# Optimization experiments

Measured on AMD Instinct MI355X. Metric: run time of the kernel, lower is better.

Reference implementation:

```python
import jax, jax.numpy as jnp
import numpy as np

N = 20000   # nodes per type per hop
E = 200000  # edges per relation per hop
H = 512     # node_feature_hid_len
FU = 512    # raw user feature len
FI = 256    # raw item feature len
NUM_RES = 2
NUM_DNN = 2


def setup_inputs() -> dict:
    key = jax.random.key(0)
    ks = iter(jax.random.split(key, 64))
    p = lambda shape: jax.random.normal(next(ks), shape, dtype=jnp.float32) * 0.05
    inp = {}
    # features per hop per type
    for h in range(3):
        inp[f'feat_user_h{h}'] = jax.random.normal(next(ks), (N, FU), dtype=jnp.float32)
        inp[f'feat_item_h{h}'] = jax.random.normal(next(ks), (N, FI), dtype=jnp.float32)
    del inp['feat_user_h2_']; 


def _unused():
    pass

# rebuild setup_inputs cleanly (above stub replaced)

def setup_inputs() -> dict:
    key = jax.random.key(0)
    ks = iter(jax.random.split(key, 64))
    p = lambda shape: jax.random.normal(next(ks), shape, dtype=jnp.float32) * 0.05
    inp = {}
    for h in range(3):
        inp[f'feat_user_h{h}'] = jax.random.normal(next(ks), (N, FU), dtype=jnp.float32)
        inp[f'feat_item_h{h}'] = jax.random.normal(next(ks), (N, FI), dtype=jnp.float32)
    for name in ('edges_UI_h0', 'edges_IU_h0', 'edges_UI_h1', 'edges_IU_h1'):
        inp[name] = jax.random.randint(next(ks), (2, E), 0, N, dtype=jnp.int32)
    # per-node-type input transforms
    inp['W_user'] = p((FU, H)); inp['b_user'] = jnp.zeros((H,), jnp.float32)
    inp['W_item'] = p((FI, H)); inp['b_item'] = jnp.zeros((H,), jnp.float32)
    # per-relation GATConv params, stacked over 2 relations [UI, IU]
    inp['gat_feat_W'] = p((2, H, H)); inp['gat_feat_b'] = jnp.zeros((2, H), jnp.float32)
    inp['gat_att_w'] = p((2, 2 * H)); inp['gat_att_b'] = jnp.zeros((2,), jnp.float32)
    inp['gat_bias'] = jnp.zeros((2, H), jnp.float32)
    # Res_DNN params
    inp['prep_W'] = p((H, H)); inp['prep_b'] = jnp.zeros((H,), jnp.float32)
    inp['dnn_W'] = p((NUM_RES, NUM_DNN, H, H)); inp['dnn_b'] = jnp.zeros((NUM_RES, NUM_DNN, H), jnp.float32)
    inp['dnn_ln_g'] = jnp.ones((NUM_RES, NUM_DNN, H), jnp.float32); inp['dnn_ln_b'] = jnp.zeros((NUM_RES, NUM_DNN, H), jnp.float32)
    inp['res_ln_g'] = jnp.ones((NUM_RES, H), jnp.float32); inp['res_ln_b'] = jnp.zeros((NUM_RES, H), jnp.float32)
    inp['cls_W'] = p((H, 1)); inp['cls_b'] = jnp.zeros((1,), jnp.float32)
    return inp


def _ln(x, g, b, eps=1e-5):
    mu = jnp.mean(x, axis=-1, keepdims=True)
    var = jnp.mean((x - mu) ** 2, axis=-1, keepdims=True)
    return (x - mu) * jax.lax.rsqrt(var + eps) * g + b


def _gat(head_h, tail_h, edges, fW, fb, aw, ab, bias):
    # GATConv: feat_linear on both sides, tanh edge attention, per-source-row
    # sparse softmax, scatter-weighted sum of transformed tail features.
    s = head_h @ fW + fb            # [Nh, H]
    t = tail_h @ fW + fb            # [Nt, H]
    src, tgt = edges[0], edges[1]
    # att(cat([s_e, t_e])) split into per-node scores (same math as concat @ aw)
    e = jnp.tanh((s @ aw[:H])[src] + (t @ aw[H:])[tgt] + ab)  # [E]
    nh = head_h.shape[0]
    m = jax.ops.segment_max(e, src, num_segments=nh)
    ex = jnp.exp(e - m[src])
    den = jax.ops.segment_sum(ex, src, num_segments=nh)
    alpha = ex / den[src]
    hp = jax.ops.segment_sum(alpha[:, None] * t[tgt], src, num_segments=nh)
    return hp + bias


def _forward(feat_user_h0, feat_item_h0, feat_user_h1, feat_item_h1,
             feat_user_h2, feat_item_h2,
             W_user, b_user, W_item, b_item,
             gat_feat_W, gat_feat_b, gat_att_w, gat_att_b, gat_bias,
             prep_W, prep_b, dnn_W, dnn_b, dnn_ln_g, dnn_ln_b,
             res_ln_g, res_ln_b, cls_W, cls_b,
             edges_UI_h0, edges_IU_h0, edges_UI_h1, edges_IU_h1):
    def gat(r, head, tail, edges):
        return _gat(head, tail, edges, gat_feat_W[r], gat_feat_b[r],
                    gat_att_w[r], gat_att_b[r], gat_bias[r])
    # hop 2 (deepest): transformed source features
    su = feat_user_h2 @ W_user + b_user
    si = feat_item_h2 @ W_item + b_item
    # hop 1
    hu = feat_user_h1 @ W_user + b_user
    hi = feat_item_h1 @ W_item + b_item
    su_new = (hu + gat(0, hu, si, edges_UI_h1)) * 0.5  # mean of [self, UI agg]
    si_new = (hi + gat(1, hi, su, edges_IU_h1)) * 0.5
    su, si = su_new, si_new
    # hop 0
    hu = feat_user_h0 @ W_user + b_user
    hi = feat_item_h0 @ W_item + b_item
    su_new = (hu + gat(0, hu, si, edges_UI_h0)) * 0.5
    su = su_new  # target node type = 'user' (first key)
    # Res_DNN head
    x = su @ prep_W + prep_b
    for r in range(NUM_RES):
        sc = x
        for d in range(NUM_DNN):
            x = _ln(jnp.tanh(x @ dnn_W[r, d] + dnn_b[r, d]), dnn_ln_g[r, d], dnn_ln_b[r, d])
        x = _ln(jnp.tanh(sc + x), res_ln_g[r], res_ln_b[r])
    return jax.nn.sigmoid(x @ cls_W + cls_b)  # [N, 1]


def reference(feat_user_h0, feat_item_h0, feat_user_h1, feat_item_h1,
              feat_user_h2, feat_item_h2,
              edges_UI_h0, edges_IU_h0, edges_UI_h1, edges_IU_h1,
              W_user, b_user, W_item, b_item,
              gat_feat_W, gat_feat_b, gat_att_w, gat_att_b, gat_bias,
              prep_W, prep_b, dnn_W, dnn_b, dnn_ln_g, dnn_ln_b,
              res_ln_g, res_ln_b, cls_W, cls_b):
    return _forward(feat_user_h0, feat_item_h0, feat_user_h1, feat_item_h1,
                    feat_user_h2, feat_item_h2,
                    W_user, b_user, W_item, b_item,
                    gat_feat_W, gat_feat_b, gat_att_w, gat_att_b, gat_bias,
                    prep_W, prep_b, dnn_W, dnn_b, dnn_ln_g, dnn_ln_b,
                    res_ln_g, res_ln_b, cls_W, cls_b,
                    edges_UI_h0, edges_IU_h0, edges_UI_h1, edges_IU_h1)
```

## Files before the change

kernel.cpp:

```cpp
#include <hip/hip_runtime.h>
#include <math.h>

#define NN 20000
#define NE 200000
#define HH 512

typedef __attribute__((ext_vector_type(8))) short short8v;
typedef __attribute__((ext_vector_type(4))) float f32x4;

__device__ inline short f2bf(float f) {
    union { float f; unsigned u; } v; v.f = f;
    unsigned r = (v.u + 0x7fffu + ((v.u >> 16) & 1u)) >> 16;
    return (short)r;
}
__device__ inline float bf2f(short s) {
    union { unsigned u; float f; } v;
    v.u = ((unsigned)(unsigned short)s) << 16;
    return v.f;
}

__device__ inline void gload_lds16(const void* g, void* l) {
    __builtin_amdgcn_global_load_lds(
        (const __attribute__((address_space(1))) void*)g,
        (__attribute__((address_space(3))) void*)l, 16, 0, 0);
}

__global__ __launch_bounds__(256)
void f2b_kernel(const float* __restrict__ src, short* __restrict__ dst, int n8)
{
    int i = blockIdx.x * 256 + threadIdx.x;
    if (i >= n8) return;
    const float4* p = (const float4*)src + (size_t)i * 2;
    float4 a = p[0], b = p[1];
    short8v s;
    s[0] = f2bf(a.x); s[1] = f2bf(a.y); s[2] = f2bf(a.z); s[3] = f2bf(a.w);
    s[4] = f2bf(b.x); s[5] = f2bf(b.y); s[6] = f2bf(b.z); s[7] = f2bf(b.w);
    ((short8v*)dst)[i] = s;
}

__global__ __launch_bounds__(256)
void wtr_kernel(const float* __restrict__ src, short* __restrict__ dst,
                int K, int Ncols)
{
    __shared__ float t[32][33];
    int bx = blockIdx.x * 32;
    int by = blockIdx.y * 32;
    int tx = threadIdx.x, ty = threadIdx.y;
    for (int i = ty; i < 32; i += 8)
        t[i][tx] = src[(size_t)(by + i) * Ncols + bx + tx];
    __syncthreads();
    for (int i = ty; i < 32; i += 8)
        dst[(size_t)(bx + i) * K + by + tx] = f2bf(t[tx][i]);
}

__global__ __launch_bounds__(256)
void mfma_lin(const short* __restrict__ X, const short* __restrict__ WT,
              const float* __restrict__ bias, float* __restrict__ outF,
              short* __restrict__ outB, int M, int K)
{
    __shared__ short8v pool[3072];

    const int tid = threadIdx.x;
    const int lane = tid & 63;
    const int w = tid >> 6;

    const int nby = (M + 127) >> 7;
    const int nwg = nby << 2;
    const int q = nwg >> 3, r = nwg & 7;
    int id = blockIdx.x;
    int xcd = id & 7, wi = id >> 3;
    int wgid = (xcd < r ? xcd * (q + 1) : r * (q + 1) + (xcd - r) * q) + wi;
    const int col0 = (wgid & 3) * 128;
    const int row0 = (wgid >> 2) * 128;

    const int wr = (w >> 1) * 64;
    const int wc = (w & 1) * 64;

    int sp0 = w * 128 + lane;
    int sp1 = sp0 + 64;
    int r0_ = sp0 >> 2, r1_ = sp1 >> 2;
    int c0_ = (sp0 & 3) ^ ((r0_ >> 1) & 3);
    int c1_ = (sp1 & 3) ^ ((r1_ >> 1) & 3);
    int ga0 = row0 + r0_; if (ga0 >= M) ga0 = M - 1;
    int ga1 = row0 + r1_; if (ga1 >= M) ga1 = M - 1;
    const short* ag0 = X + (size_t)ga0 * K + c0_ * 8;
    const short* ag1 = X + (size_t)ga1 * K + c1_ * 8;
    const short* bg0 = WT + (size_t)(col0 + r0_) * K + c0_ * 8;
    const short* bg1 = WT + (size_t)(col0 + r1_) * K + c1_ * 8;

    int ar[4], br[4];
#pragma unroll
    for (int i = 0; i < 4; ++i) {
        int rr = wr + i * 16 + (lane & 15);
        ar[i] = rr * 4 + ((lane >> 4) ^ ((rr >> 1) & 3));
        int nn = wc + i * 16 + (lane & 15);
        br[i] = nn * 4 + ((lane >> 4) ^ ((nn >> 1) & 3));
    }

    f32x4 acc[4][4];
#pragma unroll
    for (int i = 0; i < 4; ++i)
#pragma unroll
        for (int j = 0; j < 4; ++j)
            acc[i][j] = (f32x4){0.f, 0.f, 0.f, 0.f};

    auto stage = [&](int buf, int kk) {
        short8v* A = pool + buf * 512;
        short8v* B = pool + 1536 + buf * 512;
        gload_lds16(ag0 + kk, A + w * 128);
        gload_lds16(ag1 + kk, A + w * 128 + 64);
        gload_lds16(bg0 + kk, B + w * 128);
        gload_lds16(bg1 + kk, B + w * 128 + 64);
    };

    const int nt = K >> 5;
    stage(0, 0);
    if (nt > 1) stage(1, 32);
    if (nt > 2) stage(2, 64);
    int cur = 0;
    for (int t = 0; t < nt; ++t) {
        if (t + 2 < nt)      asm volatile("s_waitcnt vmcnt(8)" ::: "memory");
        else if (t + 1 < nt) asm volatile("s_waitcnt vmcnt(4)" ::: "memory");
        else                 asm volatile("s_waitcnt vmcnt(0)" ::: "memory");
        __builtin_amdgcn_s_barrier();
        const short8v* A = pool + cur * 512;
        const short8v* B = pool + 1536 + cur * 512;
        short8v af[4], bf[4];
#pragma unroll
        for (int i = 0; i < 4; ++i) af[i] = A[ar[i]];
#pragma unroll
        for (int j = 0; j < 4; ++j) bf[j] = B[br[j]];
#pragma unroll
        for (int i = 0; i < 4; ++i)
#pragma unroll
            for (int j = 0; j < 4; ++j)
                acc[i][j] = __builtin_amdgcn_mfma_f32_16x16x32_bf16(af[i], bf[j], acc[i][j], 0, 0, 0);
        __builtin_amdgcn_s_barrier();
        if (t + 3 < nt) stage(cur, (t + 3) * 32);
        cur = (cur == 2) ? 0 : cur + 1;
    }

    float bj[4];
#pragma unroll
    for (int j = 0; j < 4; ++j)
        bj[j] = bias[col0 + wc + j * 16 + (lane & 15)];

    if (outF) {
#pragma unroll
        for (int i = 0; i < 4; ++i) {
#pragma unroll
            for (int rr = 0; rr < 4; ++rr) {
                int row = row0 + wr + i * 16 + (lane >> 4) * 4 + rr;
                if (row < M) {
                    float* op = outF + (size_t)row * HH + col0 + wc + (lane & 15);
#pragma unroll
                    for (int j = 0; j < 4; ++j) op[j * 16] = acc[i][j][rr] + bj[j];
                }
            }
        }
    }
    if (outB) {
        short* lds = (short*)pool + w * 4608;
#pragma unroll
        for (int i = 0; i < 4; ++i)
#pragma unroll
            for (int rr = 0; rr < 4; ++rr) {
                int lrow = i * 16 + (lane >> 4) * 4 + rr;
#pragma unroll
                for (int j = 0; j < 4; ++j)
                    lds[lrow * 72 + j * 16 + (lane & 15)] = f2bf(acc[i][j][rr] + bj[j]);
            }
#pragma unroll
        for (int k = 0; k < 8; ++k) {
            int lr = (lane >> 3) + 8 * k;
            int lc = (lane & 7) * 8;
            int grow = row0 + wr + lr;
            if (grow < M) {
                short8v vv = *(short8v*)(lds + lr * 72 + lc);
                *(short8v*)(outB + (size_t)grow * HH + col0 + wc + lc) = vv;
            }
        }
    }
}

__global__ __launch_bounds__(256)
void gat_pre_kernel(const float* __restrict__ fW, const float* __restrict__ fb,
                    const float* __restrict__ aw, float* __restrict__ uv,
                    float* __restrict__ s0t0)
{
    int row = blockIdx.x * 4 + (threadIdx.x >> 6);
    int lane = threadIdx.x & 63;
    const float4* ah = (const float4*)aw;
    const float4* at = (const float4*)(aw + HH);
    const float4* fp;
    if (row < 512)      fp = (const float4*)(fW + (size_t)row * HH);
    else if (row == 512) fp = (const float4*)fb;
    else return;
    float du = 0.f, dv = 0.f;
#pragma unroll
    for (int l = 0; l < 2; ++l) {
        int idx = lane * 2 + l;
        float4 f = fp[idx], a = ah[idx], b = at[idx];
        du += f.x*a.x + f.y*a.y + f.z*a.z + f.w*a.w;
        dv += f.x*b.x + f.y*b.y + f.z*b.z + f.w*b.w;
    }
#pragma unroll
    for (int m = 32; m >= 1; m >>= 1) {
        du += __shfl_xor(du, m);
        dv += __shfl_xor(dv, m);
    }
    if (lane == 0) {
        if (row < 512) { uv[row] = du; uv[512 + row] = dv; }
        else           { s0t0[0] = du; s0t0[1] = dv; }
    }
}

__global__ __launch_bounds__(256)
void rowdot2_kernel(const short* __restrict__ Hd, const short* __restrict__ Tl,
                    const float* __restrict__ uv, const float* __restrict__ s0t0,
                    float* __restrict__ ss, float* __restrict__ ts, int N)
{
    int row = blockIdx.x * 4 + (threadIdx.x >> 6);
    int lane = threadIdx.x & 63;
    if (row >= N) return;
    short8v h = ((const short8v*)(Hd + (size_t)row * HH))[lane];
    short8v t = ((const short8v*)(Tl + (size_t)row * HH))[lane];
    const float4* up = (const float4*)uv + lane * 2;
    const float4* vp = (const float4*)(uv + HH) + lane * 2;
    float4 u0 = up[0], u1 = up[1], v0 = vp[0], v1 = vp[1];
    float a = bf2f(h[0])*u0.x + bf2f(h[1])*u0.y + bf2f(h[2])*u0.z + bf2f(h[3])*u0.w
            + bf2f(h[4])*u1.x + bf2f(h[5])*u1.y + bf2f(h[6])*u1.z + bf2f(h[7])*u1.w;
    float b = bf2f(t[0])*v0.x + bf2f(t[1])*v0.y + bf2f(t[2])*v0.z + bf2f(t[3])*v0.w
            + bf2f(t[4])*v1.x + bf2f(t[5])*v1.y + bf2f(t[6])*v1.z + bf2f(t[7])*v1.w;
#pragma unroll
    for (int m = 32; m >= 1; m >>= 1) {
        a += __shfl_xor(a, m);
        b += __shfl_xor(b, m);
    }
    if (lane == 0) { ss[row] = a + s0t0[0]; ts[row] = b + s0t0[1]; }
}

__global__ __launch_bounds__(256)
void count2_kernel(const int* __restrict__ s0, const int* __restrict__ s1,
                   int* __restrict__ c0, int* __restrict__ c1, int E)
{
    int i = blockIdx.x * blockDim.x + threadIdx.x;
    if (i < E) atomicAdd(&c0[s0[i]], 1);
    else if (i < 2 * E) atomicAdd(&c1[s1[i - E]], 1);
}

__global__ __launch_bounds__(1024)
void scan2_kernel(const int* __restrict__ c0, const int* __restrict__ c1,
                  int* __restrict__ o0, int* __restrict__ o1,
                  int* __restrict__ u0, int* __restrict__ u1, int n)
{
    const int* counts = blockIdx.x ? c1 : c0;
    int* offs = blockIdx.x ? o1 : o0;
    int* curs = blockIdx.x ? u1 : u0;
    __shared__ int part[1024];
    const int tid = threadIdx.x;
    const int CH = (n + 1023) / 1024;
    const int base = tid * CH;
    int s = 0;
    for (int i = 0; i < CH; ++i) {
        int idx = base + i;
        if (idx < n) s += counts[idx];
    }
    part[tid] = s;
    __syncthreads();
    for (int d = 1; d < 1024; d <<= 1) {
        int v = 0;
        if (tid >= d) v = part[tid - d];
        __syncthreads();
        if (tid >= d) part[tid] += v;
        __syncthreads();
    }
    int run = (tid == 0) ? 0 : part[tid - 1];
    for (int i = 0; i < CH; ++i) {
        int idx = base + i;
        if (idx < n) { offs[idx] = run; curs[idx] = run; run += counts[idx]; }
    }
    if (tid == 1023) offs[n] = run;
}

__global__ __launch_bounds__(256)
void fill_kernel(const int* __restrict__ src, const int* __restrict__ tgt,
                 const float* __restrict__ ss, const float* __restrict__ ts,
                 const float* __restrict__ ab_ptr, int* __restrict__ cursor,
                 int* __restrict__ tvals, float* __restrict__ wv, int E)
{
    int i = blockIdx.x * blockDim.x + threadIdx.x;
    if (i >= E) return;
    int s = src[i], t = tgt[i];
    int pos = atomicAdd(&cursor[s], 1);
    tvals[pos] = t;
    wv[pos] = expf(tanhf(ss[s] + ts[t] + ab_ptr[0]));
}

__global__ __launch_bounds__(256)
void gat_agg_kernel(const int* __restrict__ offs, const int* __restrict__ tvals,
                    const float* __restrict__ wv, const short* __restrict__ T,
                    const short* __restrict__ head, const float* __restrict__ gbias,
                    short* __restrict__ out, int N)
{
    int s = blockIdx.x * 4 + (threadIdx.x >> 6);
    int lane = threadIdx.x & 63;
    if (s >= N) return;
    const int beg = offs[s], end = offs[s + 1];
    float a[8];
#pragma unroll
    for (int q = 0; q < 8; ++q) a[q] = 0.f;
    float den = 0.f;

    int j = beg;
    for (; j + 4 <= end; j += 4) {
        int t0 = tvals[j], t1 = tvals[j + 1], t2 = tvals[j + 2], t3 = tvals[j + 3];
        float w0 = wv[j], w1 = wv[j + 1], w2 = wv[j + 2], w3 = wv[j + 3];
        short8v v0 = ((const short8v*)(T + (size_t)t0 * HH))[lane];
        short8v v1 = ((const short8v*)(T + (size_t)t1 * HH))[lane];
        short8v v2 = ((const short8v*)(T + (size_t)t2 * HH))[lane];
        short8v v3 = ((const short8v*)(T + (size_t)t3 * HH))[lane];
        den += w0 + w1 + w2 + w3;
#pragma unroll
        for (int q = 0; q < 8; ++q) {
            float acc = a[q];
            acc = fmaf(w0, bf2f(v0[q]), acc);
            acc = fmaf(w1, bf2f(v1[q]), acc);
            acc = fmaf(w2, bf2f(v2[q]), acc);
            acc = fmaf(w3, bf2f(v3[q]), acc);
            a[q] = acc;
        }
    }
    for (; j < end; ++j) {
        int t = tvals[j];
        float w = wv[j];
        short8v tv = ((const short8v*)(T + (size_t)t * HH))[lane];
        den += w;
#pragma unroll
        for (int q = 0; q < 8; ++q) a[q] = fmaf(w, bf2f(tv[q]), a[q]);
    }
    float inv = (den > 0.f) ? 1.f / den : 0.f;

    short8v h = ((const short8v*)(head + (size_t)s * HH))[lane];
    const float4* bp = (const float4*)gbias + lane * 2;
    float4 b0 = bp[0], b1 = bp[1];
    float bb[8] = {b0.x, b0.y, b0.z, b0.w, b1.x, b1.y, b1.z, b1.w};
    short8v o;
#pragma unroll
    for (int q = 0; q < 8; ++q)
        o[q] = f2bf((bf2f(h[q]) + a[q] * inv + bb[q]) * 0.5f);
    ((short8v*)(out + (size_t)s * HH))[lane] = o;
}

__global__ __launch_bounds__(256)
void tanh_ln_kernel(const short* __restrict__ Z, const float* __restrict__ res,
                    const float* __restrict__ g, const float* __restrict__ bta,
                    short* __restrict__ outB, float* __restrict__ outF,
                    const float* __restrict__ cWp, const float* __restrict__ cbp,
                    float* __restrict__ outCls, int N)
{
    int row = blockIdx.x * 4 + (threadIdx.x >> 6);
    int lane = threadIdx.x & 63;
    if (row >= N) return;
    short8v zv = ((const short8v*)(Z + (size_t)row * HH))[lane];
    float v[8];
    float sum = 0.f, sum2 = 0.f;
    float rr[8];
    if (res) {
        const float4* rp = (const float4*)(res + (size_t)row * HH) + lane * 2;
        float4 r0 = rp[0], r1 = rp[1];
        rr[0]=r0.x; rr[1]=r0.y; rr[2]=r0.z; rr[3]=r0.w;
        rr[4]=r1.x; rr[5]=r1.y; rr[6]=r1.z; rr[7]=r1.w;
    } else {
#pragma unroll
        for (int q = 0; q < 8; ++q) rr[q] = 0.f;
    }
#pragma unroll
    for (int q = 0; q < 8; ++q) {
        float t = tanhf(bf2f(zv[q]) + rr[q]);
        v[q] = t;
        sum += t;
        sum2 = fmaf(t, t, sum2);
    }
#pragma unroll
    for (int m = 32; m >= 1; m >>= 1) {
        sum  += __shfl_xor(sum, m);
        sum2 += __shfl_xor(sum2, m);
    }
    float mu  = sum * (1.f/HH);
    float var = sum2 * (1.f/HH) - mu*mu;
    float rs  = rsqrtf(var + 1e-5f);
    const float4* gp = (const float4*)g + lane * 2;
    const float4* bp = (const float4*)bta + lane * 2;
    float4 g0 = gp[0], g1 = gp[1], c0 = bp[0], c1 = bp[1];
    float gg[8] = {g0.x, g0.y, g0.z, g0.w, g1.x, g1.y, g1.z, g1.w};
    float cc[8] = {c0.x, c0.y, c0.z, c0.w, c1.x, c1.y, c1.z, c1.w};
    float o[8];
#pragma unroll
    for (int q = 0; q < 8; ++q) o[q] = (v[q]-mu)*rs*gg[q] + cc[q];
    if (outB) {
        short8v ob;
#pragma unroll
        for (int q = 0; q < 8; ++q) ob[q] = f2bf(o[q]);
        ((short8v*)(outB + (size_t)row * HH))[lane] = ob;
    }
    if (outF) {
        float4* op = (float4*)(outF + (size_t)row * HH) + lane * 2;
        op[0] = make_float4(o[0], o[1], o[2], o[3]);
        op[1] = make_float4(o[4], o[5], o[6], o[7]);
    }
    if (cWp) {
        const float4* wp = (const float4*)cWp + lane * 2;
        float4 w0 = wp[0], w1 = wp[1];
        float acc = o[0]*w0.x + o[1]*w0.y + o[2]*w0.z + o[3]*w0.w
                  + o[4]*w1.x + o[5]*w1.y + o[6]*w1.z + o[7]*w1.w;
#pragma unroll
        for (int m = 32; m >= 1; m >>= 1) acc += __shfl_xor(acc, m);
        if (lane == 0) outCls[row] = 1.f / (1.f + expf(-(acc + cbp[0])));
    }
}

extern "C" void kernel_launch(void* const* d_in, const int* in_sizes, int n_in,
                              void* d_out, int out_size, void* d_ws, size_t ws_size,
                              hipStream_t stream)
{
    (void)in_sizes; (void)n_in; (void)out_size; (void)ws_size;
    const int N = NN, E = NE, H = HH;
    const size_t NHf = (size_t)N * H;

    const float* fu0 = (const float*)d_in[0];
    const float* fi1 = (const float*)d_in[3];
    const float* fu2 = (const float*)d_in[4];
    const int* eUI0 = (const int*)d_in[6];
    const int* eIU1 = (const int*)d_in[9];
    const float* Wu  = (const float*)d_in[10];
    const float* bu  = (const float*)d_in[11];
    const float* Wi  = (const float*)d_in[12];
    const float* bi  = (const float*)d_in[13];
    const float* gfW = (const float*)d_in[14];
    const float* gfb = (const float*)d_in[15];
    const float* gaw = (const float*)d_in[16];
    const float* gab = (const float*)d_in[17];
    const float* gbias = (const float*)d_in[18];
    const float* prW = (const float*)d_in[19];
    const float* prb = (const float*)d_in[20];
    const float* dW  = (const float*)d_in[21];
    const float* db  = (const float*)d_in[22];
    const float* dlg = (const float*)d_in[23];
    const float* dlb = (const float*)d_in[24];
    const float* rlg = (const float*)d_in[25];
    const float* rlb = (const float*)d_in[26];
    const float* cW  = (const float*)d_in[27];
    const float* cb  = (const float*)d_in[28];

    float* B5   = (float*)d_ws;
    float* ssb  = B5 + NHf;
    float* tsb  = ssb + N;
    float* uv   = tsb + N;
    float* s0t0 = uv + 1024;
    float* wvb  = s0t0 + 4;
    int* counts0 = (int*)(wvb + E);
    int* counts1 = counts0 + N;
    int* offs0   = counts1 + N;
    int* offs1   = offs0 + N + 1;
    int* cur0    = offs1 + N + 1;
    int* cur1    = cur0 + N;
    int* tvals   = cur1 + N;
    size_t boff = (size_t)((char*)(tvals + E) - (char*)d_ws);
    boff = (boff + 15) & ~(size_t)15;
    short* S0    = (short*)((char*)d_ws + boff);
    short* SUHU  = S0 + 2 * NHf;
    short* XI1   = SUHU + 2 * NHf;
    short* HI    = XI1 + NHf / 2;
    short* SINEW = HI + NHf;
    short* T4    = SINEW + NHf;
    short* SUF   = T4 + NHf;
    short* WTu   = SUF + NHf;
    short* WTi   = WTu + 512 * 512;
    short* WTg0  = WTi + 512 * 256;
    short* WTg1  = WTg0 + 512 * 512;
    short* WTpr  = WTg1 + 512 * 512;
    short* WTd   = WTpr + 512 * 512;
    short* SU  = SUHU;
    short* HU0 = SUHU + NHf;
    short* XB  = SINEW;
    short* ZB  = SU;

    auto WTR = [&](const float* src, short* dst, int K) {
        hipLaunchKernelGGL(wtr_kernel, dim3(16, K / 32), dim3(32, 8), 0, stream,
                           src, dst, K, 512);
    };
    WTR(Wu, WTu, 512);
    WTR(Wi, WTi, 256);
    WTR(gfW, WTg0, 512);
    WTR(gfW + (size_t)H * H, WTg1, 512);
    WTR(prW, WTpr, 512);
    for (int k = 0; k < 4; ++k)
        WTR(dW + (size_t)k * H * H, WTd + (size_t)k * 512 * 512, 512);

    auto F2B = [&](const float* src, short* dst, size_t n) {
        int n8 = (int)(n / 8);
        hipLaunchKernelGGL(f2b_kernel, dim3((n8 + 255) / 256), dim3(256), 0, stream,
                           src, dst, n8);
    };

    hipMemsetAsync(counts0, 0, 2 * N * sizeof(int), stream);
    hipLaunchKernelGGL(count2_kernel, dim3((2 * E + 255) / 256), dim3(256), 0, stream,
                       eUI0, eIU1, counts0, counts1, E);
    hipLaunchKernelGGL(scan2_kernel, dim3(2), dim3(1024), 0, stream,
                       counts0, counts1, offs0, offs1, cur0, cur1, N);

    auto MLIN = [&](const short* X, const short* WT, const float* b,
                    float* oF, short* oB, int M, int K) {
        int nwg = ((M + 127) / 128) * 4;
        hipLaunchKernelGGL(mfma_lin, dim3(nwg), dim3(256), 0, stream,
                           X, WT, b, oF, oB, M, K);
    };
    const int rgrid = (N + 3) / 4;
    const int egrid = (E + 255) / 256;

    auto GAT = [&](int r, const short* headB, const short* tailB, const short* WTg,
                   const int* edges, int* offs, int* curs, short* outB) {
        hipLaunchKernelGGL(gat_pre_kernel, dim3(130), dim3(256), 0, stream,
                           gfW + (size_t)r * H * H, gfb + r * H, gaw + (size_t)r * 2 * H,
                           uv, s0t0);
        MLIN(tailB, WTg, gfb + r * H, nullptr, T4, N, 512);
        hipLaunchKernelGGL(rowdot2_kernel, dim3(rgrid), dim3(256), 0, stream,
                           headB, tailB, uv, s0t0, ssb, tsb, N);
        hipLaunchKernelGGL(fill_kernel, dim3(egrid), dim3(256), 0, stream,
                           edges, edges + E, ssb, tsb, gab + r, curs, tvals, wvb, E);
        hipLaunchKernelGGL(gat_agg_kernel, dim3(rgrid), dim3(256), 0, stream,
                           offs, tvals, wvb, T4, headB, gbias + (size_t)r * H, outB, N);
    };

    F2B(fu2, S0, NHf);
    F2B(fu0, S0 + NHf, NHf);
    F2B(fi1, XI1, NHf / 2);
    MLIN(S0, WTu, bu, nullptr, SUHU, 2 * N, 512);
    MLIN(XI1, WTi, bi, nullptr, HI, N, 256);
    GAT(1, HI, SU, WTg1, eIU1, offs1, cur1, SINEW);
    GAT(0, HU0, SINEW, WTg0, eUI0, offs0, cur0, SUF);

    MLIN(SUF, WTpr, prb, B5, XB, N, 512);
    for (int r = 0; r < 2; ++r) {
        for (int d = 0; d < 2; ++d) {
            MLIN(XB, WTd + (size_t)(r * 2 + d) * 512 * 512, db + (r * 2 + d) * H,
                 nullptr, ZB, N, 512);
            hipLaunchKernelGGL(tanh_ln_kernel, dim3(rgrid), dim3(256), 0, stream,
                               ZB, (const float*)nullptr, dlg + (r * 2 + d) * H,
                               dlb + (r * 2 + d) * H, XB, (float*)nullptr,
                               (const float*)nullptr, (const float*)nullptr,
                               (float*)nullptr, N);
        }
        if (r == 0) {
            hipLaunchKernelGGL(tanh_ln_kernel, dim3(rgrid), dim3(256), 0, stream,
                               XB, B5, rlg, rlb, XB, B5,
                               (const float*)nullptr, (const float*)nullptr,
                               (float*)nullptr, N);
        } else {
            hipLaunchKernelGGL(tanh_ln_kernel, dim3(rgrid), dim3(256), 0, stream,
                               XB, B5, rlg + H, rlb + H, (short*)nullptr,
                               (float*)nullptr, cW, cb, (float*)d_out, N);
        }
    }
}
```

Baseline: 571.7 us.

## Shrink GEMM tile to 128x64 with four 32-row warps for more workgroups

```diff
diff --git a/kernel.cpp b/kernel.cpp
--- a/kernel.cpp
+++ b/kernel.cpp
@@ -58,59 +58,62 @@
               const float* __restrict__ bias, float* __restrict__ outF,
               short* __restrict__ outB, int M, int K)
 {
-    __shared__ short8v pool[3072];
+    __shared__ short8v pool[2304];
 
     const int tid = threadIdx.x;
     const int lane = tid & 63;
     const int w = tid >> 6;
 
     const int nby = (M + 127) >> 7;
-    const int nwg = nby << 2;
+    const int nwg = nby << 3;
     const int q = nwg >> 3, r = nwg & 7;
     int id = blockIdx.x;
     int xcd = id & 7, wi = id >> 3;
     int wgid = (xcd < r ? xcd * (q + 1) : r * (q + 1) + (xcd - r) * q) + wi;
-    const int col0 = (wgid & 3) * 128;
-    const int row0 = (wgid >> 2) * 128;
-
-    const int wr = (w >> 1) * 64;
-    const int wc = (w & 1) * 64;
-
-    int sp0 = w * 128 + lane;
-    int sp1 = sp0 + 64;
-    int r0_ = sp0 >> 2, r1_ = sp1 >> 2;
-    int c0_ = (sp0 & 3) ^ ((r0_ >> 1) & 3);
-    int c1_ = (sp1 & 3) ^ ((r1_ >> 1) & 3);
-    int ga0 = row0 + r0_; if (ga0 >= M) ga0 = M - 1;
-    int ga1 = row0 + r1_; if (ga1 >= M) ga1 = M - 1;
-    const short* ag0 = X + (size_t)ga0 * K + c0_ * 8;
-    const short* ag1 = X + (size_t)ga1 * K + c1_ * 8;
-    const short* bg0 = WT + (size_t)(col0 + r0_) * K + c0_ * 8;
-    const short* bg1 = WT + (size_t)(col0 + r1_) * K + c1_ * 8;
-
-    int ar[4], br[4];
-#pragma unroll
-    for (int i = 0; i < 4; ++i) {
-        int rr = wr + i * 16 + (lane & 15);
+    const int col0 = (wgid & 7) * 64;
+    const int row0 = (wgid >> 3) * 128;
+
+    const short* gsrc[3];
+#pragma unroll
+    for (int g = 0; g < 3; ++g) {
+        int p = w * 192 + g * 64 + lane;
+        if (p < 512) {
+            int row = p >> 2;
+            int c = (p & 3) ^ ((row >> 1) & 3);
+            int ga = row0 + row; if (ga >= M) ga = M - 1;
+            gsrc[g] = X + (size_t)ga * K + c * 8;
+        } else {
+            int qq = p - 512;
+            int col = qq >> 2;
+            int c = (qq & 3) ^ ((col >> 1) & 3);
+            gsrc[g] = WT + (size_t)(col0 + col) * K + c * 8;
+        }
+    }
+
+    int ar[2], br[4];
+#pragma unroll
+    for (int i = 0; i < 2; ++i) {
+        int rr = w * 32 + i * 16 + (lane & 15);
         ar[i] = rr * 4 + ((lane >> 4) ^ ((rr >> 1) & 3));
-        int nn = wc + i * 16 + (lane & 15);
-        br[i] = nn * 4 + ((lane >> 4) ^ ((nn >> 1) & 3));
-    }
-
-    f32x4 acc[4][4];
-#pragma unroll
-    for (int i = 0; i < 4; ++i)
+    }
+#pragma unroll
+    for (int j = 0; j < 4; ++j) {
+        int nn = j * 16 + (lane & 15);
+        br[j] = 512 + nn * 4 + ((lane >> 4) ^ ((nn >> 1) & 3));
+    }
+
+    f32x4 acc[2][4];
+#pragma unroll
+    for (int i = 0; i < 2; ++i)
 #pragma unroll
         for (int j = 0; j < 4; ++j)
             acc[i][j] = (f32x4){0.f, 0.f, 0.f, 0.f};
 
     auto stage = [&](int buf, int kk) {
-        short8v* A = pool + buf * 512;
-        short8v* B = pool + 1536 + buf * 512;
-        gload_lds16(ag0 + kk, A + w * 128);
-        gload_lds16(ag1 + kk, A + w * 128 + 64);
-        gload_lds16(bg0 + kk, B + w * 128);
-        gload_lds16(bg1 + kk, B + w * 128 + 64);
+        short8v* base = pool + buf * 768 + w * 192;
+#pragma unroll
+        for (int g = 0; g < 3; ++g)
+            gload_lds16(gsrc[g] + kk, base + g * 64);
     };
 
     const int nt = K >> 5;
@@ -119,19 +122,18 @@
     if (nt > 2) stage(2, 64);
     int cur = 0;
     for (int t = 0; t < nt; ++t) {
-        if (t + 2 < nt)      asm volatile("s_waitcnt vmcnt(8)" ::: "memory");
-        else if (t + 1 < nt) asm volatile("s_waitcnt vmcnt(4)" ::: "memory");
+        if (t + 2 < nt)      asm volatile("s_waitcnt vmcnt(6)" ::: "memory");
+        else if (t + 1 < nt) asm volatile("s_waitcnt vmcnt(3)" ::: "memory");
         else                 asm volatile("s_waitcnt vmcnt(0)" ::: "memory");
         __builtin_amdgcn_s_barrier();
-        const short8v* A = pool + cur * 512;
-        const short8v* B = pool + 1536 + cur * 512;
-        short8v af[4], bf[4];
-#pragma unroll
-        for (int i = 0; i < 4; ++i) af[i] = A[ar[i]];
-#pragma unroll
-        for (int j = 0; j < 4; ++j) bf[j] = B[br[j]];
-#pragma unroll
-        for (int i = 0; i < 4; ++i)
+        const short8v* S = pool + cur * 768;
+        short8v af[2], bf[4];
+#pragma unroll
+        for (int i = 0; i < 2; ++i) af[i] = S[ar[i]];
+#pragma unroll
+        for (int j = 0; j < 4; ++j) bf[j] = S[br[j]];
+#pragma unroll
+        for (int i = 0; i < 2; ++i)
 #pragma unroll
             for (int j = 0; j < 4; ++j)
                 acc[i][j] = __builtin_amdgcn_mfma_f32_16x16x32_bf16(af[i], bf[j], acc[i][j], 0, 0, 0);
@@ -143,16 +145,16 @@
     float bj[4];
 #pragma unroll
     for (int j = 0; j < 4; ++j)
-        bj[j] = bias[col0 + wc + j * 16 + (lane & 15)];
+        bj[j] = bias[col0 + j * 16 + (lane & 15)];
 
     if (outF) {
 #pragma unroll
-        for (int i = 0; i < 4; ++i) {
+        for (int i = 0; i < 2; ++i) {
 #pragma unroll
             for (int rr = 0; rr < 4; ++rr) {
-                int row = row0 + wr + i * 16 + (lane >> 4) * 4 + rr;
+                int row = row0 + w * 32 + i * 16 + (lane >> 4) * 4 + rr;
                 if (row < M) {
-                    float* op = outF + (size_t)row * HH + col0 + wc + (lane & 15);
+                    float* op = outF + (size_t)row * HH + col0 + (lane & 15);
 #pragma unroll
                     for (int j = 0; j < 4; ++j) op[j * 16] = acc[i][j][rr] + bj[j];
                 }
@@ -160,9 +162,9 @@
         }
     }
     if (outB) {
-        short* lds = (short*)pool + w * 4608;
-#pragma unroll
-        for (int i = 0; i < 4; ++i)
+        short* lds = (short*)pool + w * 2304;
+#pragma unroll
+        for (int i = 0; i < 2; ++i)
 #pragma unroll
             for (int rr = 0; rr < 4; ++rr) {
                 int lrow = i * 16 + (lane >> 4) * 4 + rr;
@@ -171,13 +173,13 @@
                     lds[lrow * 72 + j * 16 + (lane & 15)] = f2bf(acc[i][j][rr] + bj[j]);
             }
 #pragma unroll
-        for (int k = 0; k < 8; ++k) {
+        for (int k = 0; k < 4; ++k) {
             int lr = (lane >> 3) + 8 * k;
             int lc = (lane & 7) * 8;
-            int grow = row0 + wr + lr;
+            int grow = row0 + w * 32 + lr;
             if (grow < M) {
                 short8v vv = *(short8v*)(lds + lr * 72 + lc);
-                *(short8v*)(outB + (size_t)grow * HH + col0 + wc + lc) = vv;
+                *(short8v*)(outB + (size_t)grow * HH + col0 + lc) = vv;
             }
         }
     }
@@ -512,7 +514,7 @@
 
     auto MLIN = [&](const short* X, const short* WT, const float* b,
                     float* oF, short* oB, int M, int K) {
-        int nwg = ((M + 127) / 128) * 4;
+        int nwg = ((M + 127) / 128) * 8;
         hipLaunchKernelGGL(mfma_lin, dim3(nwg), dim3(256), 0, stream,
                            X, WT, b, oF, oB, M, K);
     };
```

New measurement: 612.2 us. 1.07x slower.

## Switch GEMM to BK=64 tiles with double buffering instead of triple

Applied to the files above, without the earlier changes.

```diff
diff --git a/kernel.cpp b/kernel.cpp
--- a/kernel.cpp
+++ b/kernel.cpp
@@ -58,7 +58,7 @@
               const float* __restrict__ bias, float* __restrict__ outF,
               short* __restrict__ outB, int M, int K)
 {
-    __shared__ short8v pool[3072];
+    __shared__ short8v pool[4096];
 
     const int tid = threadIdx.x;
     const int lane = tid & 63;
@@ -76,25 +76,33 @@
     const int wr = (w >> 1) * 64;
     const int wc = (w & 1) * 64;
 
-    int sp0 = w * 128 + lane;
-    int sp1 = sp0 + 64;
-    int r0_ = sp0 >> 2, r1_ = sp1 >> 2;
-    int c0_ = (sp0 & 3) ^ ((r0_ >> 1) & 3);
-    int c1_ = (sp1 & 3) ^ ((r1_ >> 1) & 3);
-    int ga0 = row0 + r0_; if (ga0 >= M) ga0 = M - 1;
-    int ga1 = row0 + r1_; if (ga1 >= M) ga1 = M - 1;
-    const short* ag0 = X + (size_t)ga0 * K + c0_ * 8;
-    const short* ag1 = X + (size_t)ga1 * K + c1_ * 8;
-    const short* bg0 = WT + (size_t)(col0 + r0_) * K + c0_ * 8;
-    const short* bg1 = WT + (size_t)(col0 + r1_) * K + c1_ * 8;
-
-    int ar[4], br[4];
-#pragma unroll
-    for (int i = 0; i < 4; ++i) {
-        int rr = wr + i * 16 + (lane & 15);
-        ar[i] = rr * 4 + ((lane >> 4) ^ ((rr >> 1) & 3));
-        int nn = wc + i * 16 + (lane & 15);
-        br[i] = nn * 4 + ((lane >> 4) ^ ((nn >> 1) & 3));
+    const short* gsrc[8];
+#pragma unroll
+    for (int g = 0; g < 8; ++g) {
+        int p = w * 512 + g * 64 + lane;
+        if (p < 1024) {
+            int row = p >> 3;
+            int c = (p & 7) ^ (row & 7);
+            int ga = row0 + row; if (ga >= M) ga = M - 1;
+            gsrc[g] = X + (size_t)ga * K + c * 8;
+        } else {
+            int qq = p - 1024;
+            int col = qq >> 3;
+            int c = (qq & 7) ^ (col & 7);
+            gsrc[g] = WT + (size_t)(col0 + col) * K + c * 8;
+        }
+    }
+
+    int ar[2][4], br[2][4];
+#pragma unroll
+    for (int kk = 0; kk < 2; ++kk) {
+#pragma unroll
+        for (int i = 0; i < 4; ++i) {
+            int rr = wr + i * 16 + (lane & 15);
+            ar[kk][i] = rr * 8 + ((kk * 4 + (lane >> 4)) ^ (rr & 7));
+            int nn = wc + i * 16 + (lane & 15);
+            br[kk][i] = 1024 + nn * 8 + ((kk * 4 + (lane >> 4)) ^ (nn & 7));
+        }
     }
 
     f32x4 acc[4][4];
@@ -105,39 +113,37 @@
             acc[i][j] = (f32x4){0.f, 0.f, 0.f, 0.f};
 
     auto stage = [&](int buf, int kk) {
-        short8v* A = pool + buf * 512;
-        short8v* B = pool + 1536 + buf * 512;
-        gload_lds16(ag0 + kk, A + w * 128);
-        gload_lds16(ag1 + kk, A + w * 128 + 64);
-        gload_lds16(bg0 + kk, B + w * 128);
-        gload_lds16(bg1 + kk, B + w * 128 + 64);
+        short8v* base = pool + buf * 2048 + w * 512;
+#pragma unroll
+        for (int g = 0; g < 8; ++g)
+            gload_lds16(gsrc[g] + kk, base + g * 64);
     };
 
-    const int nt = K >> 5;
+    const int nt = K >> 6;
     stage(0, 0);
-    if (nt > 1) stage(1, 32);
-    if (nt > 2) stage(2, 64);
+    if (nt > 1) stage(1, 64);
     int cur = 0;
     for (int t = 0; t < nt; ++t) {
-        if (t + 2 < nt)      asm volatile("s_waitcnt vmcnt(8)" ::: "memory");
-        else if (t + 1 < nt) asm volatile("s_waitcnt vmcnt(4)" ::: "memory");
-        else                 asm volatile("s_waitcnt vmcnt(0)" ::: "memory");
+        if (t + 1 < nt) asm volatile("s_waitcnt vmcnt(8)" ::: "memory");
+        else            asm volatile("s_waitcnt vmcnt(0)" ::: "memory");
         __builtin_amdgcn_s_barrier();
-        const short8v* A = pool + cur * 512;
-        const short8v* B = pool + 1536 + cur * 512;
-        short8v af[4], bf[4];
-#pragma unroll
-        for (int i = 0; i < 4; ++i) af[i] = A[ar[i]];
-#pragma unroll
-        for (int j = 0; j < 4; ++j) bf[j] = B[br[j]];
-#pragma unroll
-        for (int i = 0; i < 4; ++i)
-#pragma unroll
-            for (int j = 0; j < 4; ++j)
-                acc[i][j] = __builtin_amdgcn_mfma_f32_16x16x32_bf16(af[i], bf[j], acc[i][j], 0, 0, 0);
+        const short8v* S = pool + cur * 2048;
+#pragma unroll
+        for (int kk = 0; kk < 2; ++kk) {
+            short8v af[4], bf[4];
+#pragma unroll
+            for (int i = 0; i < 4; ++i) af[i] = S[ar[kk][i]];
+#pragma unroll
+            for (int j = 0; j < 4; ++j) bf[j] = S[br[kk][j]];
+#pragma unroll
+            for (int i = 0; i < 4; ++i)
+#pragma unroll
+                for (int j = 0; j < 4; ++j)
+                    acc[i][j] = __builtin_amdgcn_mfma_f32_16x16x32_bf16(af[i], bf[j], acc[i][j], 0, 0, 0);
+        }
         __builtin_amdgcn_s_barrier();
-        if (t + 3 < nt) stage(cur, (t + 3) * 32);
-        cur = (cur == 2) ? 0 : cur + 1;
+        if (t + 2 < nt) stage(cur, (t + 2) * 64);
+        cur ^= 1;
     }
 
     float bj[4];
```

After: 561.3 us. No clear change (-1.8%).
